# Kernel optimization log

Hardware: AMD Instinct MI355X
Metric: run time of the kernel (lower is better)

The kernel has to match this reference:

```python
import jax, jax.numpy as jnp
import numpy as np
from jax import lax

BN_EPS = 1e-5
LN_EPS = 1e-5
EPS = 1e-6


def _bn(x, g, b, m, v):
    inv = g / jnp.sqrt(v + BN_EPS)
    return (x - m[None, :, None, None]) * inv[None, :, None, None] + b[None, :, None, None]


def _conv1x1(x, w, b=None):
    y = jnp.einsum('bchw,oc->bohw', x, w)
    if b is not None:
        y = y + b[None, :, None, None]
    return y


def _conv2d(x, w, pad_h, pad_w):
    return lax.conv_general_dilated(x, w, (1, 1), [(pad_h, pad_h), (pad_w, pad_w)],
                                    dimension_numbers=('NCHW', 'OIHW', 'NCHW'))


def _haar_dwt(x):
    # Haar analysis, stride-2: pure 2x2 add/sub arithmetic (H, W assumed even).
    B, C, H, W = x.shape
    xb = x.reshape(B, C, H // 2, 2, W // 2, 2)
    x00 = xb[:, :, :, 0, :, 0]; x01 = xb[:, :, :, 0, :, 1]
    x10 = xb[:, :, :, 1, :, 0]; x11 = xb[:, :, :, 1, :, 1]
    LL = 0.5 * (x00 + x01 + x10 + x11)
    LH = 0.5 * (-x00 + x01 - x10 + x11)
    HL = 0.5 * (-x00 - x01 + x10 + x11)
    HH = 0.5 * (x00 - x01 - x10 + x11)
    return LH, HL, HH, LL


def _haar_idwt(LH, HL, HH, LL):
    # Matches conv_transpose2d(stride=2) with the same Haar kernels.
    x00 = 0.5 * (LL - LH - HL + HH); x01 = 0.5 * (LL + LH - HL - HH)
    x10 = 0.5 * (LL - LH + HL - HH); x11 = 0.5 * (LL + LH + HL + HH)
    B, C, h, w = LL.shape
    top = jnp.stack([x00, x01], axis=-1)  # (B,C,h,w,2)
    bot = jnp.stack([x10, x11], axis=-1)
    y = jnp.stack([top, bot], axis=3)     # (B,C,h,2,w,2)
    return y.reshape(B, C, 2 * h, 2 * w)


def _soft_threshold(x, thr):
    return jnp.sign(x) * jax.nn.relu(jnp.abs(x) - thr)


def _forward(x, red_w, red_bias, red_bn_g, red_bn_b, red_bn_m, red_bn_v,
             gct_fc1_w, gct_fc1_b, gct_ln_g, gct_ln_b, gct_fc2_w, gct_fc2_b,
             rel_h_w, rel_h_b, rel_h_bn_g, rel_h_bn_b, rel_h_bn_m, rel_h_bn_v,
             rel_v_w, rel_v_b, rel_v_bn_g, rel_v_bn_b, rel_v_bn_m, rel_v_bn_v,
             rel_fus_w, rel_fus_b, hw_theta, hw_fuse_w, hw_fc_w, hw_fc_b,
             sf_w, sf_b, sf_bn_g, sf_bn_b, sf_bn_m, sf_bn_v, fin_w, fin_b):
    B, C, H, W = x.shape
    split = C // 2  # alpha = 0.5
    identity = x[:, :split]
    gate = x[:, split:]
    r = jax.nn.relu(_bn(_conv1x1(gate, red_w, red_bias), red_bn_g, red_bn_b, red_bn_m, red_bn_v))
    # --- GCT stream: GAP -> Linear -> LayerNorm -> ReLU -> Linear -> sigmoid gate ---
    ctx = r.mean(axis=(2, 3))                      # (B,Cr)
    h1 = ctx @ gct_fc1_w.T + gct_fc1_b
    mu = h1.mean(-1, keepdims=True)
    var = ((h1 - mu) ** 2).mean(-1, keepdims=True)
    h1 = (h1 - mu) / jnp.sqrt(var + LN_EPS) * gct_ln_g + gct_ln_b
    w_gct = jax.nn.sigmoid(jax.nn.relu(h1) @ gct_fc2_w.T + gct_fc2_b)
    gct_out = r * w_gct[:, :, None, None]
    # --- Rel stream: anisotropic pool -> conv/BN/ReLU -> bilinear(size-1 axis == broadcast) ---
    hf = _conv2d(r.mean(axis=2, keepdims=True), rel_h_w, 0, 1) + rel_h_b[None, :, None, None]
    hf = jax.nn.relu(_bn(hf, rel_h_bn_g, rel_h_bn_b, rel_h_bn_m, rel_h_bn_v))
    hf = jnp.broadcast_to(hf, (B, hf.shape[1], H, W))
    vf = _conv2d(r.mean(axis=3, keepdims=True), rel_v_w, 1, 0) + rel_v_b[None, :, None, None]
    vf = jax.nn.relu(_bn(vf, rel_v_bn_g, rel_v_bn_b, rel_v_bn_m, rel_v_bn_v))
    vf = jnp.broadcast_to(vf, (B, vf.shape[1], H, W))
    rel_w_map = jax.nn.sigmoid(_conv1x1(jnp.concatenate([hf, vf], axis=1), rel_fus_w, rel_fus_b))
    rel_out = r * rel_w_map
    # --- HWFE / wavelet attention ---
    LH, HL, HH, LL = _haar_dwt(r)
    t = jax.nn.sigmoid(hw_theta)                   # (3,Cr,1,1)
    m_LH = jnp.abs(LH).mean(axis=(2, 3), keepdims=True) + EPS
    m_HL = jnp.abs(HL).mean(axis=(2, 3), keepdims=True) + EPS
    m_HH = jnp.abs(HH).mean(axis=(2, 3), keepdims=True) + EPS
    LH_h = _soft_threshold(LH, t[0][None] * m_LH)
    HL_h = _soft_threshold(HL, t[1][None] * m_HL)
    HH_h = _soft_threshold(HH, t[2][None] * m_HH)
    fused = _conv1x1(jnp.concatenate([LH_h, HL_h, HH_h], axis=1), hw_fuse_w)
    X_re = _haar_idwt(LH_h, HL_h, fused, LL)       # note: fused sits in HH slot, as in source
    gap = X_re.mean(axis=(2, 3)) @ hw_fc_w.T + hw_fc_b
    attn = jax.nn.softmax(gap, axis=1)
    hwfe_out = r * attn[:, :, None, None]
    # --- stream fusion + gating ---
    interaction = gct_out * rel_out + hwfe_out
    gate_weight = jax.nn.sigmoid(_bn(_conv1x1(interaction, sf_w, sf_b), sf_bn_g, sf_bn_b, sf_bn_m, sf_bn_v))
    out = jnp.concatenate([identity, gate * gate_weight], axis=1)
    return _conv1x1(out, fin_w, fin_b)


def setup_inputs() -> dict:
    key = jax.random.key(0)
    ks = jax.random.split(key, 20)
    B, C, H, W = 16, 512, 64, 64
    Cg = C // 2           # gate channels = 256
    Cr = 16               # max(4, 256 // 16)
    Ch = Cr // 2          # 8
    Hd = max(1, Cr // 4)  # 4
    f = lambda k, s: jax.random.normal(k, s, jnp.float32) * 0.05
    return dict(
        x=jax.random.normal(ks[0], (B, C, H, W), jnp.float32),
        red_w=f(ks[1], (Cr, Cg)), red_bias=f(ks[2], (Cr,)),
        red_bn_g=jnp.ones((Cr,)), red_bn_b=jnp.zeros((Cr,)),
        red_bn_m=jnp.zeros((Cr,)), red_bn_v=jnp.ones((Cr,)),
        gct_fc1_w=f(ks[3], (Hd, Cr)), gct_fc1_b=f(ks[4], (Hd,)),
        gct_ln_g=jnp.ones((Hd,)), gct_ln_b=jnp.zeros((Hd,)),
        gct_fc2_w=f(ks[5], (Cr, Hd)), gct_fc2_b=f(ks[6], (Cr,)),
        rel_h_w=f(ks[7], (Ch, Cr, 1, 3)), rel_h_b=f(ks[8], (Ch,)),
        rel_h_bn_g=jnp.ones((Ch,)), rel_h_bn_b=jnp.zeros((Ch,)),
        rel_h_bn_m=jnp.zeros((Ch,)), rel_h_bn_v=jnp.ones((Ch,)),
        rel_v_w=f(ks[9], (Ch, Cr, 3, 1)), rel_v_b=f(ks[10], (Ch,)),
        rel_v_bn_g=jnp.ones((Ch,)), rel_v_bn_b=jnp.zeros((Ch,)),
        rel_v_bn_m=jnp.zeros((Ch,)), rel_v_bn_v=jnp.ones((Ch,)),
        rel_fus_w=f(ks[11], (Cr, 2 * Ch)), rel_fus_b=f(ks[12], (Cr,)),
        hw_theta=f(ks[13], (3, Cr, 1, 1)), hw_fuse_w=f(ks[14], (Cr, 3 * Cr)),
        hw_fc_w=f(ks[15], (Cr, Cr)), hw_fc_b=f(ks[16], (Cr,)),
        sf_w=f(ks[17], (Cg, Cr)), sf_b=f(ks[18], (Cg,)),
        sf_bn_g=jnp.ones((Cg,)), sf_bn_b=jnp.zeros((Cg,)),
        sf_bn_m=jnp.zeros((Cg,)), sf_bn_v=jnp.ones((Cg,)),
        fin_w=f(ks[19], (C, C)), fin_b=jnp.zeros((C,)),
    )


def reference(x, red_w, red_bias, red_bn_g, red_bn_b, red_bn_m, red_bn_v,
              gct_fc1_w, gct_fc1_b, gct_ln_g, gct_ln_b, gct_fc2_w, gct_fc2_b,
              rel_h_w, rel_h_b, rel_h_bn_g, rel_h_bn_b, rel_h_bn_m, rel_h_bn_v,
              rel_v_w, rel_v_b, rel_v_bn_g, rel_v_bn_b, rel_v_bn_m, rel_v_bn_v,
              rel_fus_w, rel_fus_b, hw_theta, hw_fuse_w, hw_fc_w, hw_fc_b,
              sf_w, sf_b, sf_bn_g, sf_bn_b, sf_bn_m, sf_bn_v, fin_w, fin_b):
    return _forward(x, red_w, red_bias, red_bn_g, red_bn_b, red_bn_m, red_bn_v,
                    gct_fc1_w, gct_fc1_b, gct_ln_g, gct_ln_b, gct_fc2_w, gct_fc2_b,
                    rel_h_w, rel_h_b, rel_h_bn_g, rel_h_bn_b, rel_h_bn_m, rel_h_bn_v,
                    rel_v_w, rel_v_b, rel_v_bn_g, rel_v_bn_b, rel_v_bn_m, rel_v_bn_v,
                    rel_fus_w, rel_fus_b, hw_theta, hw_fuse_w, hw_fc_w, hw_fc_b,
                    sf_w, sf_b, sf_bn_g, sf_bn_b, sf_bn_m, sf_bn_v, fin_w, fin_b)
```

## Files before the change

### kernel.cpp

```cpp
#include <hip/hip_runtime.h>
#include <cstdint>

typedef uint16_t u16;
typedef uint32_t u32;
typedef uint64_t u64;
typedef __attribute__((ext_vector_type(4))) float f32x4;
typedef __attribute__((ext_vector_type(8))) short bf16x8;

__device__ __forceinline__ u16 f2bf(float f) {
  union { float f; u32 i; } u; u.f = f;
  u32 r = u.i + 0x7FFFu + ((u.i >> 16) & 1u);
  return (u16)(r >> 16);
}
__device__ __forceinline__ float sigm(float x) { return 1.f / (1.f + __expf(-x)); }

__global__ __launch_bounds__(256) void k1_reduce(
    const float* __restrict__ x, const float* __restrict__ rw, const float* __restrict__ rb,
    const float* __restrict__ bg, const float* __restrict__ bb, const float* __restrict__ bm,
    const float* __restrict__ bv, float* __restrict__ r)
{
  __shared__ __align__(16) float wl[256][16];
  __shared__ float bl[16];
  __shared__ float sl[16];
  int t = threadIdx.x;
  if (t < 16) {
    float s = bg[t] * rsqrtf(bv[t] + 1e-5f);
    sl[t] = s;
    bl[t] = (rb[t] - bm[t]) * s + bb[t];
  }
  __syncthreads();
  for (int i = 0; i < 16; ++i) {
    int flat = i * 256 + t;
    int co = flat >> 8, c = flat & 255;
    wl[c][co] = rw[co * 256 + c] * sl[co];
  }
  __syncthreads();
  int p = blockIdx.x * 256 + t;
  int b = p >> 12, pp = p & 4095;
  const float* gsrc = x + ((size_t)(b * 512 + 256)) * 4096 + pp;
  float acc[16];
#pragma unroll
  for (int co = 0; co < 16; ++co) acc[co] = bl[co];
#pragma unroll 8
  for (int c = 0; c < 256; ++c) {
    float g = gsrc[(size_t)c * 4096];
    const f32x4* wr = (const f32x4*)(&wl[c][0]);
    f32x4 a0 = wr[0], a1 = wr[1], a2 = wr[2], a3 = wr[3];
    acc[0]  += g * a0[0]; acc[1]  += g * a0[1]; acc[2]  += g * a0[2]; acc[3]  += g * a0[3];
    acc[4]  += g * a1[0]; acc[5]  += g * a1[1]; acc[6]  += g * a1[2]; acc[7]  += g * a1[3];
    acc[8]  += g * a2[0]; acc[9]  += g * a2[1]; acc[10] += g * a2[2]; acc[11] += g * a2[3];
    acc[12] += g * a3[0]; acc[13] += g * a3[1]; acc[14] += g * a3[2]; acc[15] += g * a3[3];
  }
  float* rd = r + ((size_t)b * 16) * 4096 + pp;
#pragma unroll
  for (int co = 0; co < 16; ++co) rd[(size_t)co * 4096] = fmaxf(acc[co], 0.f);
}

__global__ __launch_bounds__(256) void k2_means(
    const float* __restrict__ r, float* __restrict__ cm, float* __restrict__ rm,
    float* __restrict__ ctx)
{
  __shared__ __align__(16) float tile[64][68];
  int bc = blockIdx.x, t = threadIdx.x;
  const float* src = r + (size_t)bc * 4096;
#pragma unroll
  for (int i = 0; i < 4; ++i) {
    int off = (i * 256 + t) * 4;
    int row = off >> 6, col = off & 63;
    f32x4 v = *(const f32x4*)(src + off);
    *(f32x4*)&tile[row][col] = v;
  }
  __syncthreads();
  int wv = t >> 6, lane = t & 63;
  if (wv == 0) {
    float s = 0.f;
    for (int h = 0; h < 64; ++h) s += tile[h][lane];
    cm[bc * 64 + lane] = s * (1.f / 64.f);
    float tot = s;
#pragma unroll
    for (int m = 32; m; m >>= 1) tot += __shfl_xor(tot, m, 64);
    if (lane == 0) ctx[bc] = tot * (1.f / 4096.f);
  } else if (wv == 1) {
    float s = 0.f;
    for (int w0 = 0; w0 < 64; ++w0) s += tile[lane][(w0 + lane) & 63];
    rm[bc * 64 + lane] = s * (1.f / 64.f);
  }
}

__global__ __launch_bounds__(256) void k3x(
    const float* __restrict__ finw, u16* __restrict__ fwb,
    const float* __restrict__ ctx,
    const float* f1w, const float* f1b, const float* lng, const float* lnb,
    const float* f2w, const float* f2b, const float* fcw, const float* fcb,
    float* __restrict__ wgct, float* __restrict__ attn,
    const float* __restrict__ cm, const float* __restrict__ rm,
    const float* hw, const float* hb, const float* hbg, const float* hbb, const float* hbm, const float* hbv,
    const float* vw, const float* vb_, const float* vbg, const float* vbb, const float* vbm, const float* vbv,
    const float* fw, const float* fb, float* __restrict__ hfc, float* __restrict__ vfc)
{
  int bid = blockIdx.x, t = threadIdx.x;
  if (bid < 256) {
    int i = bid * 256 + t;
    f32x4 v = ((const f32x4*)finw)[i];
    u64 p = (u64)f2bf(v[0]) | ((u64)f2bf(v[1]) << 16) |
            ((u64)f2bf(v[2]) << 32) | ((u64)f2bf(v[3]) << 48);
    ((u64*)fwb)[i] = p;
  } else if (bid == 256) {
    __shared__ float cl[256];
    __shared__ float gl[256];
    cl[t] = ctx[t];
    __syncthreads();
    int b = t >> 4, c = t & 15;
    const float* cb = &cl[b * 16];
    float a[4];
#pragma unroll
    for (int j = 0; j < 4; ++j) {
      float s = f1b[j];
      for (int i = 0; i < 16; ++i) s += cb[i] * f1w[j * 16 + i];
      a[j] = s;
    }
    float mu = 0.25f * (a[0] + a[1] + a[2] + a[3]);
    float var = 0.f;
#pragma unroll
    for (int j = 0; j < 4; ++j) { float d = a[j] - mu; var += d * d; }
    var *= 0.25f;
    float inv = rsqrtf(var + 1e-5f);
#pragma unroll
    for (int j = 0; j < 4; ++j)
      a[j] = fmaxf((a[j] - mu) * inv * lng[j] + lnb[j], 0.f);
    float s2 = f2b[c];
#pragma unroll
    for (int j = 0; j < 4; ++j) s2 += a[j] * f2w[c * 4 + j];
    wgct[t] = sigm(s2);
    float g = fcb[c];
    for (int i = 0; i < 16; ++i) g += cb[i] * fcw[c * 16 + i];
    gl[t] = g;
    __syncthreads();
    const float* gb = &gl[b * 16];
    float mx = -1e30f;
    for (int i = 0; i < 16; ++i) mx = fmaxf(mx, gb[i]);
    float den = 0.f;
    for (int i = 0; i < 16; ++i) den += __expf(gb[i] - mx);
    attn[t] = __expf(g - mx) / den;
  } else {
    __shared__ float cml[16][64], rml[16][64];
    int b = bid - 257;
#pragma unroll
    for (int i = 0; i < 4; ++i) {
      int idx = i * 256 + t;
      int row = idx >> 6, col = idx & 63;
      cml[row][col] = cm[(b * 16 + row) * 64 + col];
      rml[row][col] = rm[(b * 16 + row) * 64 + col];
    }
    __syncthreads();
    if (t < 64) {
      float hf[8], vf[8];
      for (int o = 0; o < 8; ++o) {
        float sh = 0.f, sv = 0.f;
        for (int ci = 0; ci < 16; ++ci) {
#pragma unroll
          for (int kk = 0; kk < 3; ++kk) {
            int q = t + kk - 1;
            bool ok = (q >= 0 && q < 64);
            int qi = ok ? q : 0;
            float xh = ok ? cml[ci][qi] : 0.f;
            float xv = ok ? rml[ci][qi] : 0.f;
            sh += hw[(o * 16 + ci) * 3 + kk] * xh;
            sv += vw[(o * 16 + ci) * 3 + kk] * xv;
          }
        }
        float s1 = hbg[o] * rsqrtf(hbv[o] + 1e-5f);
        hf[o] = fmaxf((sh + hb[o] - hbm[o]) * s1 + hbb[o], 0.f);
        float s2 = vbg[o] * rsqrtf(vbv[o] + 1e-5f);
        vf[o] = fmaxf((sv + vb_[o] - vbm[o]) * s2 + vbb[o], 0.f);
      }
      for (int o = 0; o < 16; ++o) {
        float sh = fb[o], sv = 0.f;
#pragma unroll
        for (int c = 0; c < 8; ++c) {
          sh += fw[o * 16 + c] * hf[c];
          sv += fw[o * 16 + 8 + c] * vf[c];
        }
        hfc[(b * 16 + o) * 64 + t] = sh;
        vfc[(b * 16 + o) * 64 + t] = sv;
      }
    }
  }
}

__global__ __launch_bounds__(512, 4) void k45_v3(
    const float* __restrict__ x, const float* __restrict__ r,
    const float* __restrict__ wgct, const float* __restrict__ attn,
    const float* __restrict__ hfc, const float* __restrict__ vfc,
    const float* __restrict__ sfw, const float* __restrict__ sfb,
    const float* __restrict__ sg, const float* __restrict__ sb_,
    const float* __restrict__ sbm, const float* __restrict__ sbv,
    const u16* __restrict__ fwb, const float* __restrict__ fb,
    float* __restrict__ out)
{
  __shared__ __align__(16) u16 A[64 * 520];
  char* Ab = (char*)A;

  int bid = blockIdx.x;
  int b = bid >> 6, h = bid & 63;
  int t = threadIdx.x;
  int lane = t & 63, wv = t >> 6;

  if (t < 256) {
    int o = t;
    float s = sg[o] * rsqrtf(sbv[o] + 1e-5f);
    const f32x4* sw = (const f32x4*)(sfw + o * 16);
    f32x4 w0 = sw[0] * s, w1 = sw[1] * s, w2 = sw[2] * s, w3 = sw[3] * s;
    f32x4* wrow = (f32x4*)(Ab + (o & 63) * 1040 + 512 + (o >> 6) * 64);
    wrow[0] = w0; wrow[1] = w1; wrow[2] = w2; wrow[3] = w3;
    *(float*)(Ab + (o & 63) * 1040 + 768 + (o >> 6) * 4) =
        (sfb[o] - sbm[o]) * s + sb_[o];
  }
#pragma unroll
  for (int i = 0; i < 2; ++i) {
    int idx = i * 512 + t;
    int k = idx >> 6, w = idx & 63;
    float rv = r[((size_t)(b * 16 + k)) * 4096 + h * 64 + w];
    float rel = sigm(hfc[(b * 16 + k) * 64 + w] + vfc[(b * 16 + k) * 64 + h]);
    *(float*)(Ab + w * 1040 + 784 + k * 4) =
        rv * rv * wgct[b * 16 + k] * rel + rv * attn[b * 16 + k];
  }
  __syncthreads();

  {
    int w = t & 63, og = t >> 6;
    const char* irow = Ab + w * 1040 + 784;
    f32x4 iv0 = *(const f32x4*)(irow);
    f32x4 iv1 = *(const f32x4*)(irow + 16);
    f32x4 iv2 = *(const f32x4*)(irow + 32);
    f32x4 iv3 = *(const f32x4*)(irow + 48);
    const float* gsrc = x + ((size_t)(b * 512 + 256)) * 4096 + h * 64 + w;
#pragma unroll
    for (int jo = 0; jo < 4; ++jo) {
      bf16x8 vb;
#pragma unroll
      for (int jj = 0; jj < 8; ++jj) {
        int o = og * 32 + jo * 8 + jj;
        const char* orow = Ab + (o & 63) * 1040;
        const f32x4* wr = (const f32x4*)(orow + 512 + (o >> 6) * 64);
        f32x4 w0 = wr[0], w1 = wr[1], w2 = wr[2], w3 = wr[3];
        float dot = *(const float*)(orow + 768 + (o >> 6) * 4);
        dot += iv0[0] * w0[0] + iv0[1] * w0[1] + iv0[2] * w0[2] + iv0[3] * w0[3];
        dot += iv1[0] * w1[0] + iv1[1] * w1[1] + iv1[2] * w1[2] + iv1[3] * w1[3];
        dot += iv2[0] * w2[0] + iv2[1] * w2[1] + iv2[2] * w2[2] + iv2[3] * w2[3];
        dot += iv3[0] * w3[0] + iv3[1] * w3[1] + iv3[2] * w3[2] + iv3[3] * w3[3];
        float gwv = sigm(dot);
        float gv = gsrc[(size_t)o * 4096];
        vb[jj] = (short)f2bf(gv * gwv);
      }
      *(bf16x8*)(Ab + w * 1040 + (og * 32 + jo * 8) * 2) = vb;
    }
  }
  __syncthreads();

  {
    int q = lane & 15, cg = lane >> 4;
    int qp = lane & 15, jp = lane >> 4;
    int m = qp * 4 + jp;
#pragma unroll
    for (int i = 0; i < 8; ++i) {
      int c = i * 32 + wv * 4 + cg;
      f32x4 v = *(const f32x4*)(x + ((size_t)(b * 512 + c)) * 4096 + h * 64 + q * 4);
      u32 w01 = (u32)f2bf(v[0]) | ((u32)f2bf(v[1]) << 16);
      u32 w23 = (u32)f2bf(v[2]) | ((u32)f2bf(v[3]) << 16);
      u32 e[4];
#pragma unroll
      for (int cp = 0; cp < 4; ++cp) {
        int srcaddr = (cp * 16 + qp) << 2;
        u32 r01 = (u32)__builtin_amdgcn_ds_bpermute(srcaddr, (int)w01);
        u32 r23 = (u32)__builtin_amdgcn_ds_bpermute(srcaddr, (int)w23);
        u32 sel = (jp < 2) ? r01 : r23;
        e[cp] = (jp & 1) ? (sel >> 16) : (sel & 0xffffu);
      }
      u64 pk = (u64)e[0] | ((u64)e[1] << 16) | ((u64)e[2] << 32) | ((u64)e[3] << 48);
      *(u64*)(Ab + m * 1040 + 512 + (i * 32 + wv * 4) * 2) = pk;
    }
  }
  __syncthreads();

  int fr = lane & 15, quad = lane >> 4;
  int n0w = wv * 64;
  f32x4 acc[4][4];
#pragma unroll
  for (int j = 0; j < 4; ++j) {
    float bvv = fb[n0w + j * 16 + fr];
    f32x4 b4 = {bvv, bvv, bvv, bvv};
#pragma unroll
    for (int i = 0; i < 4; ++i) acc[i][j] = b4;
  }
  const u16* Bp = fwb + (size_t)(n0w + fr) * 512 + quad * 8;
  for (int kb = 0; kb < 16; ++kb) {
    int c0 = kb * 32 + quad * 8;
    int kbb = kb ^ 8;
    bf16x8 af[4], bfr[4];
#pragma unroll
    for (int i = 0; i < 4; ++i)
      af[i] = *(const bf16x8*)(A + (i * 16 + fr) * 520 + c0);
#pragma unroll
    for (int j = 0; j < 4; ++j)
      bfr[j] = *(const bf16x8*)(Bp + (size_t)(j * 16) * 512 + kbb * 32);
#pragma unroll
    for (int j = 0; j < 4; ++j)
#pragma unroll
      for (int i = 0; i < 4; ++i)
        acc[i][j] = __builtin_amdgcn_mfma_f32_16x16x32_bf16(af[i], bfr[j], acc[i][j], 0, 0, 0);
  }

  float* ob = out + ((size_t)(b * 512 + n0w + fr)) * 4096 + h * 64 + quad * 4;
#pragma unroll
  for (int j = 0; j < 4; ++j)
#pragma unroll
    for (int i = 0; i < 4; ++i)
      *(f32x4*)(ob + (size_t)(j * 16) * 4096 + i * 16) = acc[i][j];
}

extern "C" void kernel_launch(void* const* d_in, const int* in_sizes, int n_in,
                              void* d_out, int out_size, void* d_ws, size_t ws_size,
                              hipStream_t stream) {
  const float* x      = (const float*)d_in[0];
  const float* red_w  = (const float*)d_in[1];
  const float* red_b  = (const float*)d_in[2];
  const float* rbg    = (const float*)d_in[3];
  const float* rbb    = (const float*)d_in[4];
  const float* rbm    = (const float*)d_in[5];
  const float* rbv    = (const float*)d_in[6];
  const float* f1w    = (const float*)d_in[7];
  const float* f1b    = (const float*)d_in[8];
  const float* lng    = (const float*)d_in[9];
  const float* lnb    = (const float*)d_in[10];
  const float* f2w    = (const float*)d_in[11];
  const float* f2b    = (const float*)d_in[12];
  const float* rhw    = (const float*)d_in[13];
  const float* rhb    = (const float*)d_in[14];
  const float* rhbg   = (const float*)d_in[15];
  const float* rhbb   = (const float*)d_in[16];
  const float* rhbm   = (const float*)d_in[17];
  const float* rhbv   = (const float*)d_in[18];
  const float* rvw    = (const float*)d_in[19];
  const float* rvb    = (const float*)d_in[20];
  const float* rvbg   = (const float*)d_in[21];
  const float* rvbb   = (const float*)d_in[22];
  const float* rvbm   = (const float*)d_in[23];
  const float* rvbv   = (const float*)d_in[24];
  const float* fusw   = (const float*)d_in[25];
  const float* fusb   = (const float*)d_in[26];
  const float* fcw    = (const float*)d_in[29];
  const float* fcb    = (const float*)d_in[30];
  const float* sfw    = (const float*)d_in[31];
  const float* sfb    = (const float*)d_in[32];
  const float* sbg    = (const float*)d_in[33];
  const float* sbb    = (const float*)d_in[34];
  const float* sbm    = (const float*)d_in[35];
  const float* sbv    = (const float*)d_in[36];
  const float* finw   = (const float*)d_in[37];
  const float* finb   = (const float*)d_in[38];
  float* out = (float*)d_out;

  char* ws = (char*)d_ws;
  size_t off = 0;
  float* r   = (float*)(ws + off); off += (size_t)16 * 16 * 4096 * 4;
  u16*   fwb = (u16*)(ws + off);   off += (size_t)512 * 512 * 2;
  float* cm  = (float*)(ws + off); off += 65536;
  float* rm  = (float*)(ws + off); off += 65536;
  float* ctx = (float*)(ws + off); off += 1024;
  float* wg  = (float*)(ws + off); off += 1024;
  float* at  = (float*)(ws + off); off += 1024;
  float* hfc = (float*)(ws + off); off += 65536;
  float* vfc = (float*)(ws + off); off += 65536;

  k1_reduce<<<256, 256, 0, stream>>>(x, red_w, red_b, rbg, rbb, rbm, rbv, r);
  k2_means<<<256, 256, 0, stream>>>(r, cm, rm, ctx);
  k3x<<<273, 256, 0, stream>>>(finw, fwb,
                               ctx, f1w, f1b, lng, lnb, f2w, f2b, fcw, fcb, wg, at,
                               cm, rm, rhw, rhb, rhbg, rhbb, rhbm, rhbv,
                               rvw, rvb, rvbg, rvbb, rvbm, rvbv, fusw, fusb, hfc, vfc);
  k45_v3<<<1024, 512, 0, stream>>>(x, r, wg, at, hfc, vfc,
                                   sfw, sfb, sbg, sbb, sbm, sbv, fwb, finb, out);
}
```

Before: 423.5 us.

## Split k1 channel reduction across waves and XOR-swizzle k45 shared memory

k1_reduce now splits the 256-channel reduction across four waves, each handling 64 channels for 64 pixels. Partial sums are combined through shared memory, and the grid grows from 256 to 1024 blocks to raise occupancy and memory parallelism. k45 pads its LDS rows to 1056 bytes and XOR-swizzles addresses by row to reduce bank conflicts on the MFMA A-fragment and gating loads. The x-transpose stage now writes 16-byte packed stores covering 8 channels. The changes add an extra LDS reduction pass in k1 and more complex address arithmetic.

Measured after the change: 401.1 us. -5.3%, faster.

```diff
diff --git a/kernel.cpp b/kernel.cpp
--- a/kernel.cpp
+++ b/kernel.cpp
@@ -14,7 +14,7 @@
 }
 __device__ __forceinline__ float sigm(float x) { return 1.f / (1.f + __expf(-x)); }
 
-__global__ __launch_bounds__(256) void k1_reduce(
+__global__ __launch_bounds__(256, 4) void k1_reduce(
     const float* __restrict__ x, const float* __restrict__ rw, const float* __restrict__ rb,
     const float* __restrict__ bg, const float* __restrict__ bb, const float* __restrict__ bm,
     const float* __restrict__ bv, float* __restrict__ r)
@@ -22,6 +22,7 @@
   __shared__ __align__(16) float wl[256][16];
   __shared__ float bl[16];
   __shared__ float sl[16];
+  __shared__ float sc[4][64][17];
   int t = threadIdx.x;
   if (t < 16) {
     float s = bg[t] * rsqrtf(bv[t] + 1e-5f);
@@ -35,25 +36,34 @@
     wl[c][co] = rw[co * 256 + c] * sl[co];
   }
   __syncthreads();
-  int p = blockIdx.x * 256 + t;
-  int b = p >> 12, pp = p & 4095;
-  const float* gsrc = x + ((size_t)(b * 512 + 256)) * 4096 + pp;
+  int g = t >> 6, l = t & 63;
+  int pg = blockIdx.x * 64 + l;
+  int b = pg >> 12, pp = pg & 4095;
+  const float* gsrc = x + ((size_t)(b * 512 + 256 + g * 64)) * 4096 + pp;
   float acc[16];
 #pragma unroll
-  for (int co = 0; co < 16; ++co) acc[co] = bl[co];
+  for (int co = 0; co < 16; ++co) acc[co] = 0.f;
 #pragma unroll 8
-  for (int c = 0; c < 256; ++c) {
-    float g = gsrc[(size_t)c * 4096];
-    const f32x4* wr = (const f32x4*)(&wl[c][0]);
+  for (int c = 0; c < 64; ++c) {
+    float gv = gsrc[(size_t)c * 4096];
+    const f32x4* wr = (const f32x4*)(&wl[g * 64 + c][0]);
     f32x4 a0 = wr[0], a1 = wr[1], a2 = wr[2], a3 = wr[3];
-    acc[0]  += g * a0[0]; acc[1]  += g * a0[1]; acc[2]  += g * a0[2]; acc[3]  += g * a0[3];
-    acc[4]  += g * a1[0]; acc[5]  += g * a1[1]; acc[6]  += g * a1[2]; acc[7]  += g * a1[3];
-    acc[8]  += g * a2[0]; acc[9]  += g * a2[1]; acc[10] += g * a2[2]; acc[11] += g * a2[3];
-    acc[12] += g * a3[0]; acc[13] += g * a3[1]; acc[14] += g * a3[2]; acc[15] += g * a3[3];
-  }
-  float* rd = r + ((size_t)b * 16) * 4096 + pp;
-#pragma unroll
-  for (int co = 0; co < 16; ++co) rd[(size_t)co * 4096] = fmaxf(acc[co], 0.f);
+    acc[0]  += gv * a0[0]; acc[1]  += gv * a0[1]; acc[2]  += gv * a0[2]; acc[3]  += gv * a0[3];
+    acc[4]  += gv * a1[0]; acc[5]  += gv * a1[1]; acc[6]  += gv * a1[2]; acc[7]  += gv * a1[3];
+    acc[8]  += gv * a2[0]; acc[9]  += gv * a2[1]; acc[10] += gv * a2[2]; acc[11] += gv * a2[3];
+    acc[12] += gv * a3[0]; acc[13] += gv * a3[1]; acc[14] += gv * a3[2]; acc[15] += gv * a3[3];
+  }
+#pragma unroll
+  for (int co = 0; co < 16; ++co) sc[g][l][co] = acc[co];
+  __syncthreads();
+  int ppb = (blockIdx.x * 64) & 4095;
+#pragma unroll
+  for (int i = 0; i < 4; ++i) {
+    int idx = i * 256 + t;
+    int l2 = idx & 63, co = idx >> 6;
+    float s = sc[0][l2][co] + sc[1][l2][co] + sc[2][l2][co] + sc[3][l2][co] + bl[co];
+    r[((size_t)(b * 16 + co)) * 4096 + ppb + l2] = fmaxf(s, 0.f);
+  }
 }
 
 __global__ __launch_bounds__(256) void k2_means(
@@ -188,7 +198,7 @@
   }
 }
 
-__global__ __launch_bounds__(512, 4) void k45_v3(
+__global__ __launch_bounds__(512, 4) void k45_v4(
     const float* __restrict__ x, const float* __restrict__ r,
     const float* __restrict__ wgct, const float* __restrict__ attn,
     const float* __restrict__ hfc, const float* __restrict__ vfc,
@@ -198,7 +208,7 @@
     const u16* __restrict__ fwb, const float* __restrict__ fb,
     float* __restrict__ out)
 {
-  __shared__ __align__(16) u16 A[64 * 520];
+  __shared__ __align__(16) u16 A[64 * 528];
   char* Ab = (char*)A;
 
   int bid = blockIdx.x;
@@ -208,12 +218,14 @@
 
   if (t < 256) {
     int o = t;
+    int orow = o & 63, ov = (orow & 7) << 4, ohi = o >> 6;
     float s = sg[o] * rsqrtf(sbv[o] + 1e-5f);
     const f32x4* sw = (const f32x4*)(sfw + o * 16);
-    f32x4 w0 = sw[0] * s, w1 = sw[1] * s, w2 = sw[2] * s, w3 = sw[3] * s;
-    f32x4* wrow = (f32x4*)(Ab + (o & 63) * 1040 + 512 + (o >> 6) * 64);
-    wrow[0] = w0; wrow[1] = w1; wrow[2] = w2; wrow[3] = w3;
-    *(float*)(Ab + (o & 63) * 1040 + 768 + (o >> 6) * 4) =
+    char* rbase = Ab + orow * 1056;
+#pragma unroll
+    for (int j = 0; j < 4; ++j)
+      *(f32x4*)(rbase + ((512 + ohi * 64 + j * 16) ^ ov)) = sw[j] * s;
+    *(float*)(rbase + ((768 + ohi * 4) ^ ov)) =
         (sfb[o] - sbm[o]) * s + sb_[o];
   }
 #pragma unroll
@@ -222,18 +234,19 @@
     int k = idx >> 6, w = idx & 63;
     float rv = r[((size_t)(b * 16 + k)) * 4096 + h * 64 + w];
     float rel = sigm(hfc[(b * 16 + k) * 64 + w] + vfc[(b * 16 + k) * 64 + h]);
-    *(float*)(Ab + w * 1040 + 784 + k * 4) =
+    *(float*)(Ab + w * 1056 + ((784 + k * 4) ^ ((w & 7) << 4))) =
         rv * rv * wgct[b * 16 + k] * rel + rv * attn[b * 16 + k];
   }
   __syncthreads();
 
   {
     int w = t & 63, og = t >> 6;
-    const char* irow = Ab + w * 1040 + 784;
-    f32x4 iv0 = *(const f32x4*)(irow);
-    f32x4 iv1 = *(const f32x4*)(irow + 16);
-    f32x4 iv2 = *(const f32x4*)(irow + 32);
-    f32x4 iv3 = *(const f32x4*)(irow + 48);
+    int wx = (w & 7) << 4;
+    const char* irow = Ab + w * 1056;
+    f32x4 iv0 = *(const f32x4*)(irow + ((784 +  0) ^ wx));
+    f32x4 iv1 = *(const f32x4*)(irow + ((784 + 16) ^ wx));
+    f32x4 iv2 = *(const f32x4*)(irow + ((784 + 32) ^ wx));
+    f32x4 iv3 = *(const f32x4*)(irow + ((784 + 48) ^ wx));
     const float* gsrc = x + ((size_t)(b * 512 + 256)) * 4096 + h * 64 + w;
 #pragma unroll
     for (int jo = 0; jo < 4; ++jo) {
@@ -241,10 +254,13 @@
 #pragma unroll
       for (int jj = 0; jj < 8; ++jj) {
         int o = og * 32 + jo * 8 + jj;
-        const char* orow = Ab + (o & 63) * 1040;
-        const f32x4* wr = (const f32x4*)(orow + 512 + (o >> 6) * 64);
-        f32x4 w0 = wr[0], w1 = wr[1], w2 = wr[2], w3 = wr[3];
-        float dot = *(const float*)(orow + 768 + (o >> 6) * 4);
+        int orow = o & 63, ov = (orow & 7) << 4, ohi = o >> 6;
+        const char* rbase = Ab + orow * 1056;
+        f32x4 w0 = *(const f32x4*)(rbase + ((512 + ohi * 64 +  0) ^ ov));
+        f32x4 w1 = *(const f32x4*)(rbase + ((512 + ohi * 64 + 16) ^ ov));
+        f32x4 w2 = *(const f32x4*)(rbase + ((512 + ohi * 64 + 32) ^ ov));
+        f32x4 w3 = *(const f32x4*)(rbase + ((512 + ohi * 64 + 48) ^ ov));
+        float dot = *(const float*)(rbase + ((768 + ohi * 4) ^ ov));
         dot += iv0[0] * w0[0] + iv0[1] * w0[1] + iv0[2] * w0[2] + iv0[3] * w0[3];
         dot += iv1[0] * w1[0] + iv1[1] * w1[1] + iv1[2] * w1[2] + iv1[3] * w1[3];
         dot += iv2[0] * w2[0] + iv2[1] * w2[1] + iv2[2] * w2[2] + iv2[3] * w2[3];
@@ -253,37 +269,48 @@
         float gv = gsrc[(size_t)o * 4096];
         vb[jj] = (short)f2bf(gv * gwv);
       }
-      *(bf16x8*)(Ab + w * 1040 + (og * 32 + jo * 8) * 2) = vb;
+      *(bf16x8*)(Ab + w * 1056 + ((og * 64 + jo * 16) ^ wx)) = vb;
     }
   }
   __syncthreads();
 
   {
     int q = lane & 15, cg = lane >> 4;
-    int qp = lane & 15, jp = lane >> 4;
-    int m = qp * 4 + jp;
-#pragma unroll
-    for (int i = 0; i < 8; ++i) {
-      int c = i * 32 + wv * 4 + cg;
-      f32x4 v = *(const f32x4*)(x + ((size_t)(b * 512 + c)) * 4096 + h * 64 + q * 4);
-      u32 w01 = (u32)f2bf(v[0]) | ((u32)f2bf(v[1]) << 16);
-      u32 w23 = (u32)f2bf(v[2]) | ((u32)f2bf(v[3]) << 16);
-      u32 e[4];
+    int m = q * 4 + cg;
+    int mx = (m & 7) << 4;
+#pragma unroll
+    for (int i = 0; i < 4; ++i) {
+      int cbase = i * 64 + wv * 8;
+      f32x4 vA = *(const f32x4*)(x + ((size_t)(b * 512 + cbase + cg)) * 4096 + h * 64 + q * 4);
+      f32x4 vB = *(const f32x4*)(x + ((size_t)(b * 512 + cbase + 4 + cg)) * 4096 + h * 64 + q * 4);
+      u32 a01 = (u32)f2bf(vA[0]) | ((u32)f2bf(vA[1]) << 16);
+      u32 a23 = (u32)f2bf(vA[2]) | ((u32)f2bf(vA[3]) << 16);
+      u32 b01 = (u32)f2bf(vB[0]) | ((u32)f2bf(vB[1]) << 16);
+      u32 b23 = (u32)f2bf(vB[2]) | ((u32)f2bf(vB[3]) << 16);
+      int jp = cg;
+      u32 e[8];
 #pragma unroll
       for (int cp = 0; cp < 4; ++cp) {
-        int srcaddr = (cp * 16 + qp) << 2;
-        u32 r01 = (u32)__builtin_amdgcn_ds_bpermute(srcaddr, (int)w01);
-        u32 r23 = (u32)__builtin_amdgcn_ds_bpermute(srcaddr, (int)w23);
-        u32 sel = (jp < 2) ? r01 : r23;
-        e[cp] = (jp & 1) ? (sel >> 16) : (sel & 0xffffu);
+        int srcaddr = (cp * 16 + q) << 2;
+        u32 rA01 = (u32)__builtin_amdgcn_ds_bpermute(srcaddr, (int)a01);
+        u32 rA23 = (u32)__builtin_amdgcn_ds_bpermute(srcaddr, (int)a23);
+        u32 rB01 = (u32)__builtin_amdgcn_ds_bpermute(srcaddr, (int)b01);
+        u32 rB23 = (u32)__builtin_amdgcn_ds_bpermute(srcaddr, (int)b23);
+        u32 selA = (jp < 2) ? rA01 : rA23;
+        u32 selB = (jp < 2) ? rB01 : rB23;
+        e[cp]     = (jp & 1) ? (selA >> 16) : (selA & 0xffffu);
+        e[4 + cp] = (jp & 1) ? (selB >> 16) : (selB & 0xffffu);
       }
-      u64 pk = (u64)e[0] | ((u64)e[1] << 16) | ((u64)e[2] << 32) | ((u64)e[3] << 48);
-      *(u64*)(Ab + m * 1040 + 512 + (i * 32 + wv * 4) * 2) = pk;
+      bf16x8 pk;
+#pragma unroll
+      for (int j = 0; j < 8; ++j) pk[j] = (short)e[j];
+      *(bf16x8*)(Ab + m * 1056 + ((512 + i * 128 + wv * 16) ^ mx)) = pk;
     }
   }
   __syncthreads();
 
   int fr = lane & 15, quad = lane >> 4;
+  int fx = (fr & 7) << 4;
   int n0w = wv * 64;
   f32x4 acc[4][4];
 #pragma unroll
@@ -295,12 +322,12 @@
   }
   const u16* Bp = fwb + (size_t)(n0w + fr) * 512 + quad * 8;
   for (int kb = 0; kb < 16; ++kb) {
-    int c0 = kb * 32 + quad * 8;
     int kbb = kb ^ 8;
     bf16x8 af[4], bfr[4];
 #pragma unroll
     for (int i = 0; i < 4; ++i)
-      af[i] = *(const bf16x8*)(A + (i * 16 + fr) * 520 + c0);
+      af[i] = *(const bf16x8*)(Ab + (size_t)(i * 16 + fr) * 1056 +
+                               ((kb * 64 + quad * 16) ^ fx));
 #pragma unroll
     for (int j = 0; j < 4; ++j)
       bfr[j] = *(const bf16x8*)(Bp + (size_t)(j * 16) * 512 + kbb * 32);
@@ -373,12 +400,12 @@
   float* hfc = (float*)(ws + off); off += 65536;
   float* vfc = (float*)(ws + off); off += 65536;
 
-  k1_reduce<<<256, 256, 0, stream>>>(x, red_w, red_b, rbg, rbb, rbm, rbv, r);
+  k1_reduce<<<1024, 256, 0, stream>>>(x, red_w, red_b, rbg, rbb, rbm, rbv, r);
   k2_means<<<256, 256, 0, stream>>>(r, cm, rm, ctx);
   k3x<<<273, 256, 0, stream>>>(finw, fwb,
                                ctx, f1w, f1b, lng, lnb, f2w, f2b, fcw, fcb, wg, at,
                                cm, rm, rhw, rhb, rhbg, rhbb, rhbm, rhbv,
                                rvw, rvb, rvbg, rvbb, rvbm, rvbv, fusw, fusb, hfc, vfc);
-  k45_v3<<<1024, 512, 0, stream>>>(x, r, wg, at, hfc, vfc,
+  k45_v4<<<1024, 512, 0, stream>>>(x, r, wg, at, hfc, vfc,
                                    sfw, sfb, sbg, sbb, sbm, sbv, fwb, finb, out);
 }
```
